# Kernel tuning notes

Hardware: AMD Instinct MI355X
Metric: run time of the kernel (lower is better)

Reference implementation:

```python
import jax, jax.numpy as jnp
import numpy as np

CTX, H, ENC, BALL = 256, 128, 128, 2
IN_DIM = 2 + BALL + ENC  # prev_disp(2) + ball(2) + encoding(128)
B, T = 8192, 128


def setup_inputs() -> dict:
    key = jax.random.key(0)
    ks = jax.random.split(key, 16)
    s = lambda fan_in: 1.0 / np.sqrt(fan_in)
    inp = {
        "context": jax.random.normal(ks[0], (B, CTX), jnp.float32),
        "target_encoding": jax.random.normal(ks[1], (B, ENC), jnp.float32),
        "ball_land_xy": jax.random.normal(ks[2], (B, BALL), jnp.float32),
        "max_frames": T,
        # context_to_h / context_to_c
        "Wh": jax.random.uniform(ks[3], (H, CTX), jnp.float32, -s(CTX), s(CTX)),
        "bh": jax.random.uniform(ks[4], (H,), jnp.float32, -s(CTX), s(CTX)),
        "Wc": jax.random.uniform(ks[5], (H, CTX), jnp.float32, -s(CTX), s(CTX)),
        "bc": jax.random.uniform(ks[6], (H,), jnp.float32, -s(CTX), s(CTX)),
        # LSTM (PyTorch gate order: i, f, g, o)
        "W_ih": jax.random.uniform(ks[7], (4 * H, IN_DIM), jnp.float32, -s(H), s(H)),
        "W_hh": jax.random.uniform(ks[8], (4 * H, H), jnp.float32, -s(H), s(H)),
        "b_ih": jax.random.uniform(ks[9], (4 * H,), jnp.float32, -s(H), s(H)),
        "b_hh": jax.random.uniform(ks[10], (4 * H,), jnp.float32, -s(H), s(H)),
        # output head
        "Wo": jax.random.uniform(ks[11], (2, H), jnp.float32, -s(H), s(H)),
        "bo": jax.random.uniform(ks[12], (2,), jnp.float32, -s(H), s(H)),
    }
    return inp


def _decode(context, target_encoding, ball_land_xy, Wh, bh, Wc, bc,
            W_ih, W_hh, b_ih, b_hh, Wo, bo, max_frames):
    h0 = context @ Wh.T + bh                      # (B, H)
    c0 = context @ Wc.T + bc                      # (B, H)
    Bn = context.shape[0]
    # split input weights: first 2 cols act on prev_disp, rest on static [ball, enc]
    W_prev = W_ih[:, :2]                          # (4H, 2)
    W_stat = W_ih[:, 2:]                          # (4H, BALL+ENC)
    static_in = jnp.concatenate([ball_land_xy, target_encoding], axis=-1)
    gate_static = static_in @ W_stat.T + b_ih + b_hh  # (B, 4H), constant per step
    Hn = h0.shape[-1]

    def step(carry, _):
        h, c, prev = carry
        gates = prev @ W_prev.T + h @ W_hh.T + gate_static
        i, f, g, o = jnp.split(gates, 4, axis=-1)
        c = jax.nn.sigmoid(f) * c + jax.nn.sigmoid(i) * jnp.tanh(g)
        h = jax.nn.sigmoid(o) * jnp.tanh(c)
        pred = h @ Wo.T + bo                      # (B, 2)
        prev = jax.lax.stop_gradient(pred)        # matches .detach()
        return (h, c, prev), pred

    prev0 = jnp.zeros((Bn, 2), dtype=context.dtype)
    _, preds = jax.lax.scan(step, (h0, c0, prev0), None, length=max_frames)
    return jnp.transpose(preds, (1, 0, 2))        # (B, T, 2)


def reference(context, target_encoding, ball_land_xy, max_frames,
              Wh, bh, Wc, bc, W_ih, W_hh, b_ih, b_hh, Wo, bo):
    return _decode(context, target_encoding, ball_land_xy, Wh, bh, Wc, bc,
                   W_ih, W_hh, b_ih, b_hh, Wo, bo, max_frames)
```

## Files before the change

### kernel.cpp

```cpp
#include <hip/hip_runtime.h>
#include <hip/hip_bf16.h>


#define HDIM 128
#define CTX_DIM 256
#define T_FRAMES 128
#define BB 32
#define STR 136

typedef __bf16 bf16x8 __attribute__((ext_vector_type(8)));
typedef float  f32x4  __attribute__((ext_vector_type(4)));

union frag_u {
  bf16x8 v;
  unsigned short s[8];
  uint4 u4;
};

#if __has_builtin(__builtin_amdgcn_exp2f)
#define EXP2(x) __builtin_amdgcn_exp2f(x)
#else
#define EXP2(x) __expf((x) * 0.6931471805599453f)
#endif
#define RCP(x) __builtin_amdgcn_rcpf(x)

__device__ __forceinline__ unsigned short f2bf(float x) {
  unsigned u = __builtin_bit_cast(unsigned, x);
  u += 0x7FFFu + ((u >> 16) & 1u);
  return (unsigned short)(u >> 16);
}
__device__ __forceinline__ float bf2f(unsigned short h) {
  unsigned u = ((unsigned)h) << 16;
  return __builtin_bit_cast(float, u);
}
template<int CTRL>
__device__ __forceinline__ float dpp_mov(float x) {
  return __builtin_bit_cast(float,
    __builtin_amdgcn_mov_dpp(__builtin_bit_cast(int, x), CTRL, 0xF, 0xF, true));
}
__device__ __forceinline__ float row_reduce16(float v) {
  v += dpp_mov<0xB1>(v);
  v += dpp_mov<0x4E>(v);
  v += dpp_mov<0x124>(v);
  v += dpp_mov<0x128>(v);
  return v;
}

template<int N> struct Int { static constexpr int value = N; };

#define MFMA(a, b, c) __builtin_amdgcn_mfma_f32_16x16x32_bf16((a), (b), (c), 0, 0, 0)

__global__ __launch_bounds__(512, 1) void traj_lstm(
    const float* __restrict__ ctx, const float* __restrict__ enc,
    const float* __restrict__ ball,
    const float* __restrict__ Wh, const float* __restrict__ bh,
    const float* __restrict__ Wc, const float* __restrict__ bc,
    const float* __restrict__ W_ih, const float* __restrict__ W_hh,
    const float* __restrict__ b_ih, const float* __restrict__ b_hh,
    const float* __restrict__ Wo, const float* __restrict__ bo,
    float* __restrict__ outp)
{
  __shared__ __align__(16) __bf16 sh_h[2][BB * STR];
  __shared__ __align__(16) unsigned short sh_sA[BB * 264];
  __shared__ __align__(16) unsigned short sh_sB[BB * 264];
  __shared__ __align__(16) uint4 sh_wof[4 * 64];
  __shared__ float sh_pw0[8][BB * 2];
  __shared__ float sh_p0[BB * 2];

  const int tid  = threadIdx.x;
  const int w    = tid >> 6;
  const int l    = tid & 63;
  const int q    = l >> 4;
  const int c16  = l & 15;
  const int colH = w * 16 + c16;
  const int rbase = blockIdx.x * BB;

  const float Lc = 1.4426950408889634f;
  const float SG[4] = {Lc, Lc, 2.f * Lc, Lc};
  const float bo0 = bo[0], bo1 = bo[1];
  const float wo0 = Wo[colH], wo1 = Wo[HDIM + colH];

  float wp0[4], wp1[4];
  #pragma unroll
  for (int g = 0; g < 4; ++g) {
    wp0[g] = W_ih[(size_t)(g * HDIM + colH) * 132 + 0];
    wp1[g] = W_ih[(size_t)(g * HDIM + colH) * 132 + 1];
  }

  frag_u Wf[4][4];
  #pragma unroll
  for (int kt = 0; kt < 4; ++kt) {
    const float* w0p = Wo + kt * 32 + q * 8;
    const float* w1p = Wo + HDIM + kt * 32 + q * 8;
    float4 a0 = *(const float4*)w0p, a1 = *(const float4*)(w0p + 4);
    float4 b0 = *(const float4*)w1p, b1 = *(const float4*)(w1p + 4);
    float wo0v[8] = {a0.x, a0.y, a0.z, a0.w, a1.x, a1.y, a1.z, a1.w};
    float wo1v[8] = {b0.x, b0.y, b0.z, b0.w, b1.x, b1.y, b1.z, b1.w};
    #pragma unroll
    for (int g = 0; g < 4; ++g) {
      const float* wr = W_hh + (size_t)(g * HDIM + colH) * HDIM + kt * 32 + q * 8;
      float4 f0 = *(const float4*)wr;
      float4 f1 = *(const float4*)(wr + 4);
      float ff[8] = {f0.x, f0.y, f0.z, f0.w, f1.x, f1.y, f1.z, f1.w};
      #pragma unroll
      for (int j = 0; j < 8; ++j)
        Wf[g][kt].s[j] = f2bf(SG[g] * (ff[j] + wp0[g] * wo0v[j] + wp1[g] * wo1v[j]));
    }
  }

  #pragma unroll
  for (int kt = 0; kt < 4; ++kt) {
    frag_u wf;
    #pragma unroll
    for (int j = 0; j < 8; ++j) {
      float x = (c16 < 2) ? Wo[c16 * HDIM + kt * 32 + q * 8 + j] : 0.f;
      wf.s[j] = f2bf(x);
    }
    if (w == 0) sh_wof[kt * 64 + l] = wf.u4;
  }

  for (int e = tid; e < BB * 256; e += 512) {
    int row = e >> 8, col = e & 255;
    float x = ctx[(size_t)(rbase + row) * CTX_DIM + col];
    unsigned short hb = f2bf(x);
    sh_sA[row * 264 + col] = hb;
    sh_sB[row * 264 + col] = f2bf(x - bf2f(hb));
  }
  __syncthreads();

  float cst[2][4];
  {
    f32x4 aH[2] = {{0.f,0.f,0.f,0.f},{0.f,0.f,0.f,0.f}};
    f32x4 aC[2] = {{0.f,0.f,0.f,0.f},{0.f,0.f,0.f,0.f}};
    #pragma unroll
    for (int kt = 0; kt < 8; ++kt) {
      frag_u Ahi[2], Alo[2];
      #pragma unroll
      for (int rt = 0; rt < 2; ++rt) {
        Ahi[rt].u4 = *(const uint4*)&sh_sA[(rt * 16 + c16) * 264 + kt * 32 + q * 8];
        Alo[rt].u4 = *(const uint4*)&sh_sB[(rt * 16 + c16) * 264 + kt * 32 + q * 8];
      }
      frag_u bhi, blo;
      {
        const float* wr = Wh + (size_t)colH * CTX_DIM + kt * 32 + q * 8;
        float4 f0 = *(const float4*)wr;
        float4 f1 = *(const float4*)(wr + 4);
        float ff[8] = {f0.x, f0.y, f0.z, f0.w, f1.x, f1.y, f1.z, f1.w};
        #pragma unroll
        for (int j = 0; j < 8; ++j) {
          unsigned short hb = f2bf(ff[j]);
          bhi.s[j] = hb;
          blo.s[j] = f2bf(ff[j] - bf2f(hb));
        }
      }
      #pragma unroll
      for (int rt = 0; rt < 2; ++rt) {
        aH[rt] = MFMA(Ahi[rt].v, bhi.v, aH[rt]);
        aH[rt] = MFMA(Alo[rt].v, bhi.v, aH[rt]);
        aH[rt] = MFMA(Ahi[rt].v, blo.v, aH[rt]);
      }
      {
        const float* wr = Wc + (size_t)colH * CTX_DIM + kt * 32 + q * 8;
        float4 f0 = *(const float4*)wr;
        float4 f1 = *(const float4*)(wr + 4);
        float ff[8] = {f0.x, f0.y, f0.z, f0.w, f1.x, f1.y, f1.z, f1.w};
        #pragma unroll
        for (int j = 0; j < 8; ++j) {
          unsigned short hb = f2bf(ff[j]);
          bhi.s[j] = hb;
          blo.s[j] = f2bf(ff[j] - bf2f(hb));
        }
      }
      #pragma unroll
      for (int rt = 0; rt < 2; ++rt) {
        aC[rt] = MFMA(Ahi[rt].v, bhi.v, aC[rt]);
        aC[rt] = MFMA(Alo[rt].v, bhi.v, aC[rt]);
        aC[rt] = MFMA(Ahi[rt].v, blo.v, aC[rt]);
      }
    }
    float bhv = bh[colH], bcv = bc[colH];
    float pp0[8][2];
    #pragma unroll
    for (int rt = 0; rt < 2; ++rt) {
      #pragma unroll
      for (int r = 0; r < 4; ++r) {
        float h0v = aH[rt][r] + bhv;
        cst[rt][r] = aC[rt][r] + bcv;
        sh_h[0][(rt * 16 + q * 4 + r) * STR + colH] = (__bf16)h0v;
        pp0[rt * 4 + r][0] = h0v * wo0;
        pp0[rt * 4 + r][1] = h0v * wo1;
      }
    }
    #pragma unroll
    for (int m = 0; m < 8; ++m) {
      pp0[m][0] = row_reduce16(pp0[m][0]);
      pp0[m][1] = row_reduce16(pp0[m][1]);
    }
    if (c16 == 0) {
      #pragma unroll
      for (int rt = 0; rt < 2; ++rt)
        #pragma unroll
        for (int r = 0; r < 4; ++r) {
          sh_pw0[w][(rt * 16 + q * 4 + r) * 2 + 0] = pp0[rt * 4 + r][0];
          sh_pw0[w][(rt * 16 + q * 4 + r) * 2 + 1] = pp0[rt * 4 + r][1];
        }
    }
  }
  __syncthreads();

  for (int e = tid; e < BB * 168; e += 512) {
    int row = e / 168, col = e - row * 168;
    float x = (col < 2) ? ball[(size_t)(rbase + row) * 2 + col]
            : (col < 130) ? enc[(size_t)(rbase + row) * 128 + (col - 2)] : 0.f;
    unsigned short hb = f2bf(x);
    sh_sA[row * 168 + col] = hb;
    sh_sB[row * 168 + col] = f2bf(x - bf2f(hb));
  }
  if (tid < BB * 2) {
    float s = (tid & 1) ? bo1 : bo0;
    #pragma unroll
    for (int w2 = 0; w2 < 8; ++w2) s += sh_pw0[w2][tid];
    sh_p0[tid] = s;
  }
  __syncthreads();

  f32x4 gacc[2][4] = {{{0.f,0.f,0.f,0.f},{0.f,0.f,0.f,0.f},{0.f,0.f,0.f,0.f},{0.f,0.f,0.f,0.f}},
                      {{0.f,0.f,0.f,0.f},{0.f,0.f,0.f,0.f},{0.f,0.f,0.f,0.f},{0.f,0.f,0.f,0.f}}};
  #pragma unroll
  for (int kt = 0; kt < 5; ++kt) {
    frag_u Ahi[2], Alo[2];
    #pragma unroll
    for (int rt = 0; rt < 2; ++rt) {
      Ahi[rt].u4 = *(const uint4*)&sh_sA[(rt * 16 + c16) * 168 + kt * 32 + q * 8];
      Alo[rt].u4 = *(const uint4*)&sh_sB[(rt * 16 + c16) * 168 + kt * 32 + q * 8];
    }
    #pragma unroll
    for (int g = 0; g < 4; ++g) {
      frag_u bhi, blo;
      #pragma unroll
      for (int j = 0; j < 8; ++j) {
        int kk = kt * 32 + q * 8 + j;
        float x = (kk < 130) ? SG[g] * W_ih[(size_t)(g * HDIM + colH) * 132 + 2 + kk] : 0.f;
        unsigned short hb = f2bf(x);
        bhi.s[j] = hb;
        blo.s[j] = f2bf(x - bf2f(hb));
      }
      #pragma unroll
      for (int rt = 0; rt < 2; ++rt) {
        gacc[rt][g] = MFMA(Ahi[rt].v, bhi.v, gacc[rt][g]);
        gacc[rt][g] = MFMA(Alo[rt].v, bhi.v, gacc[rt][g]);
        gacc[rt][g] = MFMA(Ahi[rt].v, blo.v, gacc[rt][g]);
      }
    }
  }
  float wps0[4], wps1[4];
  #pragma unroll
  for (int g = 0; g < 4; ++g) {
    int colG = g * HDIM + colH;
    float bb = SG[g] * (b_ih[colG] + b_hh[colG] + bo0 * wp0[g] + bo1 * wp1[g]);
    #pragma unroll
    for (int rt = 0; rt < 2; ++rt)
      #pragma unroll
      for (int r = 0; r < 4; ++r) gacc[rt][g][r] += bb;
    wps0[g] = SG[g] * wp0[g];
    wps1[g] = SG[g] * wp1[g];
  }

  f32x4 acc[2][4];

  auto phase = [&](auto GC, int t, bool doEw, bool corr, bool doPred) {
    constexpr int G = decltype(GC)::value;
    constexpr int E = 1 - G;
    const int rbuf = t & 1;
    const __bf16* hp = &sh_h[rbuf][(G * 16 + c16) * STR];

    frag_u A[4];
    #pragma unroll
    for (int kt = 0; kt < 4; ++kt)
      A[kt].u4 = *(const uint4*)(hp + kt * 32 + q * 8);
    #pragma unroll
    for (int g = 0; g < 4; ++g) acc[G][g] = gacc[G][g];
    #pragma unroll
    for (int kt = 0; kt < 4; ++kt)
      #pragma unroll
      for (int g = 0; g < 4; ++g)
        acc[G][g] = MFMA(A[kt].v, Wf[g][kt].v, acc[G][g]);

    if (doPred && w == 6 + G) {
      f32x4 accP = {0.f, 0.f, 0.f, 0.f};
      #pragma unroll
      for (int kt = 0; kt < 4; ++kt) {
        frag_u wof;
        wof.u4 = sh_wof[kt * 64 + l];
        accP = MFMA(A[kt].v, wof.v, accP);
      }
      if (c16 < 2) {
        const int m0 = G * 16 + q * 4;
        const float bov = c16 ? bo1 : bo0;
        #pragma unroll
        for (int r = 0; r < 4; ++r)
          outp[(size_t)(rbase + m0 + r) * (T_FRAMES * 2) + (t - 1) * 2 + c16] = accP[r] + bov;
      }
    }

    if (doEw) {
      if (corr) {
        #pragma unroll
        for (int r = 0; r < 4; ++r) {
          float2 p0r = *(const float2*)&sh_p0[(E * 16 + q * 4 + r) * 2];
          #pragma unroll
          for (int g = 0; g < 4; ++g)
            acc[E][g][r] -= p0r.x * wps0[g] + p0r.y * wps1[g];
        }
      }
      __bf16* hwp = &sh_h[(t + G) & 1][(E * 16) * STR + colH];
      #pragma unroll
      for (int r = 0; r < 4; ++r) {
        float ei = EXP2(-acc[E][0][r]);
        float ef = EXP2(-acc[E][1][r]);
        float eg = EXP2(-acc[E][2][r]);
        float eo = EXP2(-acc[E][3][r]);
        float t1 = (1.f + ei) * (1.f + eg);
        float pf = 1.f + ef;
        float num = cst[E][r] * t1 + (1.f - eg) * pf;
        float cv = num * RCP(t1 * pf);
        cst[E][r] = cv;
        float cc = fmaxf(cv, -15.f);
        float ec = EXP2(cc * (-2.f * 1.4426950408889634f));
        float hv = (1.f - ec) * RCP((1.f + eo) * (1.f + ec));
        hwp[(q * 4 + r) * STR] = (__bf16)hv;
      }
    }
    __syncthreads();
  };

  phase(Int<0>{}, 0, false, false, false);
  phase(Int<1>{}, 0, true,  true,  false);
  phase(Int<0>{}, 1, true,  true,  true);
  for (int t = 1; t < 127; ++t) {
    phase(Int<1>{}, t,     true, false, true);
    phase(Int<0>{}, t + 1, true, false, true);
  }
  phase(Int<1>{}, 127, true, false, true);

  {
    __bf16* hwp = &sh_h[0][16 * STR + colH];
    #pragma unroll
    for (int r = 0; r < 4; ++r) {
      float ei = EXP2(-acc[1][0][r]);
      float ef = EXP2(-acc[1][1][r]);
      float eg = EXP2(-acc[1][2][r]);
      float eo = EXP2(-acc[1][3][r]);
      float t1 = (1.f + ei) * (1.f + eg);
      float pf = 1.f + ef;
      float num = cst[1][r] * t1 + (1.f - eg) * pf;
      float cv = num * RCP(t1 * pf);
      float cc = fmaxf(cv, -15.f);
      float ec = EXP2(cc * (-2.f * 1.4426950408889634f));
      float hv = (1.f - ec) * RCP((1.f + eo) * (1.f + ec));
      hwp[(q * 4 + r) * STR] = (__bf16)hv;
    }
  }
  __syncthreads();

  if (w == 6 || w == 7) {
    const int Ge = w - 6;
    const __bf16* hp = &sh_h[0][(Ge * 16 + c16) * STR];
    f32x4 accP = {0.f, 0.f, 0.f, 0.f};
    #pragma unroll
    for (int kt = 0; kt < 4; ++kt) {
      frag_u A, wof;
      A.u4 = *(const uint4*)(hp + kt * 32 + q * 8);
      wof.u4 = sh_wof[kt * 64 + l];
      accP = MFMA(A.v, wof.v, accP);
    }
    if (c16 < 2) {
      const int m0 = Ge * 16 + q * 4;
      const float bov = c16 ? bo1 : bo0;
      #pragma unroll
      for (int r = 0; r < 4; ++r)
        outp[(size_t)(rbase + m0 + r) * (T_FRAMES * 2) + 127 * 2 + c16] = accP[r] + bov;
    }
  }
}

extern "C" void kernel_launch(void* const* d_in, const int* in_sizes, int n_in,
                              void* d_out, int out_size, void* d_ws, size_t ws_size,
                              hipStream_t stream) {
  (void)in_sizes; (void)n_in; (void)d_ws; (void)ws_size; (void)out_size;
  const float* ctx  = (const float*)d_in[0];
  const float* enc  = (const float*)d_in[1];
  const float* ball = (const float*)d_in[2];
  const float* Wh   = (const float*)d_in[4];
  const float* bh   = (const float*)d_in[5];
  const float* Wc   = (const float*)d_in[6];
  const float* bc   = (const float*)d_in[7];
  const float* W_ih = (const float*)d_in[8];
  const float* W_hh = (const float*)d_in[9];
  const float* b_ih = (const float*)d_in[10];
  const float* b_hh = (const float*)d_in[11];
  const float* Wo   = (const float*)d_in[12];
  const float* bo   = (const float*)d_in[13];
  float* outp = (float*)d_out;

  dim3 grid(256), block(512);
  traj_lstm<<<grid, block, 0, stream>>>(ctx, enc, ball, Wh, bh, Wc, bc,
                                        W_ih, W_hh, b_ih, b_hh, Wo, bo, outp);
}
```

Baseline: 307.1 us.

## Specialize waves into MFMA producers and elementwise consumers via LDS gate buffers

Splits the 8 waves of each block by role. Waves 0-3 hold twice the W_hh fragments and compute all gate MFMAs for one 16-row half, writing the gate sums to padded LDS buffers. Waves 4-7 read those sums, add the static gate term and run the LSTM cell math, keeping the cell state in registers. The goal is to overlap matrix and transcendental work across waves, cut per-wave register use so launch_bounds can allow 2 blocks per CU, and reuse the context staging area for the gate buffers. The cost is an extra LDS round trip for the gates at every step, a single h buffer, and load imbalance between the two roles.

```diff
diff --git a/kernel.cpp b/kernel.cpp
--- a/kernel.cpp
+++ b/kernel.cpp
@@ -7,6 +7,7 @@
 #define T_FRAMES 128
 #define BB 32
 #define STR 136
+#define GPAD 129
 
 typedef __bf16 bf16x8 __attribute__((ext_vector_type(8)));
 typedef float  f32x4  __attribute__((ext_vector_type(4)));
@@ -50,7 +51,7 @@
 
 #define MFMA(a, b, c) __builtin_amdgcn_mfma_f32_16x16x32_bf16((a), (b), (c), 0, 0, 0)
 
-__global__ __launch_bounds__(512, 1) void traj_lstm(
+__global__ __launch_bounds__(512, 2) void traj_lstm(
     const float* __restrict__ ctx, const float* __restrict__ enc,
     const float* __restrict__ ball,
     const float* __restrict__ Wh, const float* __restrict__ bh,
@@ -60,12 +61,18 @@
     const float* __restrict__ Wo, const float* __restrict__ bo,
     float* __restrict__ outp)
 {
-  __shared__ __align__(16) __bf16 sh_h[2][BB * STR];
-  __shared__ __align__(16) unsigned short sh_sA[BB * 264];
-  __shared__ __align__(16) unsigned short sh_sB[BB * 264];
+  __shared__ __align__(16) char sh_arena[2 * 16 * GPAD * 16];
+  __shared__ __align__(16) float sh_cb[BB * HDIM];
+  __shared__ __align__(16) __bf16 sh_h[BB * STR];
   __shared__ __align__(16) uint4 sh_wof[4 * 64];
   __shared__ float sh_pw0[8][BB * 2];
   __shared__ float sh_p0[BB * 2];
+
+  unsigned short* sh_sA = (unsigned short*)sh_arena;
+  unsigned short* sh_sB = sh_sA + BB * 264;
+  f32x4* gs  = (f32x4*)sh_arena;
+  f32x4* gbA = (f32x4*)sh_arena;
+  f32x4* gbB = (f32x4*)(sh_arena + 16 * GPAD * 16);
 
   const int tid  = threadIdx.x;
   const int w    = tid >> 6;
@@ -75,6 +82,9 @@
   const int colH = w * 16 + c16;
   const int rbase = blockIdx.x * BB;
 
+  const int hcE   = ((w - 4) << 5) + (l & 31);
+  const int halfE = l >> 5;
+
   const float Lc = 1.4426950408889634f;
   const float SG[4] = {Lc, Lc, 2.f * Lc, Lc};
   const float bo0 = bo[0], bo1 = bo[1];
@@ -85,27 +95,6 @@
   for (int g = 0; g < 4; ++g) {
     wp0[g] = W_ih[(size_t)(g * HDIM + colH) * 132 + 0];
     wp1[g] = W_ih[(size_t)(g * HDIM + colH) * 132 + 1];
-  }
-
-  frag_u Wf[4][4];
-  #pragma unroll
-  for (int kt = 0; kt < 4; ++kt) {
-    const float* w0p = Wo + kt * 32 + q * 8;
-    const float* w1p = Wo + HDIM + kt * 32 + q * 8;
-    float4 a0 = *(const float4*)w0p, a1 = *(const float4*)(w0p + 4);
-    float4 b0 = *(const float4*)w1p, b1 = *(const float4*)(w1p + 4);
-    float wo0v[8] = {a0.x, a0.y, a0.z, a0.w, a1.x, a1.y, a1.z, a1.w};
-    float wo1v[8] = {b0.x, b0.y, b0.z, b0.w, b1.x, b1.y, b1.z, b1.w};
-    #pragma unroll
-    for (int g = 0; g < 4; ++g) {
-      const float* wr = W_hh + (size_t)(g * HDIM + colH) * HDIM + kt * 32 + q * 8;
-      float4 f0 = *(const float4*)wr;
-      float4 f1 = *(const float4*)(wr + 4);
-      float ff[8] = {f0.x, f0.y, f0.z, f0.w, f1.x, f1.y, f1.z, f1.w};
-      #pragma unroll
-      for (int j = 0; j < 8; ++j)
-        Wf[g][kt].s[j] = f2bf(SG[g] * (ff[j] + wp0[g] * wo0v[j] + wp1[g] * wo1v[j]));
-    }
   }
 
   #pragma unroll
@@ -128,7 +117,6 @@
   }
   __syncthreads();
 
-  float cst[2][4];
   {
     f32x4 aH[2] = {{0.f,0.f,0.f,0.f},{0.f,0.f,0.f,0.f}};
     f32x4 aC[2] = {{0.f,0.f,0.f,0.f},{0.f,0.f,0.f,0.f}};
@@ -184,9 +172,10 @@
     for (int rt = 0; rt < 2; ++rt) {
       #pragma unroll
       for (int r = 0; r < 4; ++r) {
+        int row = rt * 16 + q * 4 + r;
         float h0v = aH[rt][r] + bhv;
-        cst[rt][r] = aC[rt][r] + bcv;
-        sh_h[0][(rt * 16 + q * 4 + r) * STR + colH] = (__bf16)h0v;
+        sh_h[row * STR + colH] = (__bf16)h0v;
+        sh_cb[row * HDIM + colH] = aC[rt][r] + bcv;
         pp0[rt * 4 + r][0] = h0v * wo0;
         pp0[rt * 4 + r][1] = h0v * wo1;
       }
@@ -253,7 +242,6 @@
       }
     }
   }
-  float wps0[4], wps1[4];
   #pragma unroll
   for (int g = 0; g < 4; ++g) {
     int colG = g * HDIM + colH;
@@ -262,73 +250,139 @@
     for (int rt = 0; rt < 2; ++rt)
       #pragma unroll
       for (int r = 0; r < 4; ++r) gacc[rt][g][r] += bb;
-    wps0[g] = SG[g] * wp0[g];
-    wps1[g] = SG[g] * wp1[g];
-  }
-
-  f32x4 acc[2][4];
-
-  auto phase = [&](auto GC, int t, bool doEw, bool corr, bool doPred) {
+  }
+  __syncthreads();
+
+  #pragma unroll
+  for (int rt = 0; rt < 2; ++rt)
+    #pragma unroll
+    for (int r = 0; r < 4; ++r) {
+      f32x4 vv = {gacc[rt][0][r], gacc[rt][1][r], gacc[rt][2][r], gacc[rt][3][r]};
+      gs[(rt * 16 + q * 4 + r) * HDIM + colH] = vv;
+    }
+  __syncthreads();
+
+  f32x4 gstatE[2][8];
+  float cstE[2][8];
+  float wpsE0[4], wpsE1[4];
+  frag_u Wf[4][2][4];
+  if (w >= 4) {
+    #pragma unroll
+    for (int G2 = 0; G2 < 2; ++G2)
+      #pragma unroll
+      for (int r = 0; r < 8; ++r) {
+        int row = G2 * 16 + halfE * 8 + r;
+        gstatE[G2][r] = gs[row * HDIM + hcE];
+        cstE[G2][r]   = sh_cb[row * HDIM + hcE];
+      }
+    #pragma unroll
+    for (int g = 0; g < 4; ++g) {
+      wpsE0[g] = SG[g] * W_ih[(size_t)(g * HDIM + hcE) * 132 + 0];
+      wpsE1[g] = SG[g] * W_ih[(size_t)(g * HDIM + hcE) * 132 + 1];
+    }
+  } else {
+    #pragma unroll
+    for (int ctl = 0; ctl < 2; ++ctl) {
+      const int colW = w * 32 + ctl * 16 + c16;
+      float wpA[4], wpB[4];
+      #pragma unroll
+      for (int g = 0; g < 4; ++g) {
+        wpA[g] = W_ih[(size_t)(g * HDIM + colW) * 132 + 0];
+        wpB[g] = W_ih[(size_t)(g * HDIM + colW) * 132 + 1];
+      }
+      #pragma unroll
+      for (int kt = 0; kt < 4; ++kt) {
+        const float* w0p = Wo + kt * 32 + q * 8;
+        const float* w1p = Wo + HDIM + kt * 32 + q * 8;
+        float4 a0 = *(const float4*)w0p, a1 = *(const float4*)(w0p + 4);
+        float4 b0 = *(const float4*)w1p, b1 = *(const float4*)(w1p + 4);
+        float wo0v[8] = {a0.x, a0.y, a0.z, a0.w, a1.x, a1.y, a1.z, a1.w};
+        float wo1v[8] = {b0.x, b0.y, b0.z, b0.w, b1.x, b1.y, b1.z, b1.w};
+        #pragma unroll
+        for (int g = 0; g < 4; ++g) {
+          const float* wr = W_hh + (size_t)(g * HDIM + colW) * HDIM + kt * 32 + q * 8;
+          float4 f0 = *(const float4*)wr;
+          float4 f1 = *(const float4*)(wr + 4);
+          float ff[8] = {f0.x, f0.y, f0.z, f0.w, f1.x, f1.y, f1.z, f1.w};
+          #pragma unroll
+          for (int j = 0; j < 8; ++j)
+            Wf[g][ctl][kt].s[j] = f2bf(SG[g] * (ff[j] + wpA[g] * wo0v[j] + wpB[g] * wo1v[j]));
+        }
+      }
+    }
+  }
+  __syncthreads();
+
+  auto phase = [&](auto GC, int t, bool doEW, bool corr, bool doPred) {
     constexpr int G = decltype(GC)::value;
     constexpr int E = 1 - G;
-    const int rbuf = t & 1;
-    const __bf16* hp = &sh_h[rbuf][(G * 16 + c16) * STR];
-
-    frag_u A[4];
-    #pragma unroll
-    for (int kt = 0; kt < 4; ++kt)
-      A[kt].u4 = *(const uint4*)(hp + kt * 32 + q * 8);
-    #pragma unroll
-    for (int g = 0; g < 4; ++g) acc[G][g] = gacc[G][g];
-    #pragma unroll
-    for (int kt = 0; kt < 4; ++kt)
+    if (w < 4) {
+      frag_u A[4];
+      #pragma unroll
+      for (int kt = 0; kt < 4; ++kt)
+        A[kt].u4 = *(const uint4*)&sh_h[(G * 16 + c16) * STR + kt * 32 + q * 8];
+      f32x4 acc[4][2];
       #pragma unroll
       for (int g = 0; g < 4; ++g)
-        acc[G][g] = MFMA(A[kt].v, Wf[g][kt].v, acc[G][g]);
-
-    if (doPred && w == 6 + G) {
-      f32x4 accP = {0.f, 0.f, 0.f, 0.f};
-      #pragma unroll
-      for (int kt = 0; kt < 4; ++kt) {
-        frag_u wof;
-        wof.u4 = sh_wof[kt * 64 + l];
-        accP = MFMA(A[kt].v, wof.v, accP);
-      }
-      if (c16 < 2) {
-        const int m0 = G * 16 + q * 4;
-        const float bov = c16 ? bo1 : bo0;
-        #pragma unroll
-        for (int r = 0; r < 4; ++r)
-          outp[(size_t)(rbase + m0 + r) * (T_FRAMES * 2) + (t - 1) * 2 + c16] = accP[r] + bov;
-      }
-    }
-
-    if (doEw) {
-      if (corr) {
+        #pragma unroll
+        for (int ctl = 0; ctl < 2; ++ctl)
+          acc[g][ctl] = (f32x4){0.f, 0.f, 0.f, 0.f};
+      #pragma unroll
+      for (int kt = 0; kt < 4; ++kt)
+        #pragma unroll
+        for (int g = 0; g < 4; ++g)
+          #pragma unroll
+          for (int ctl = 0; ctl < 2; ++ctl)
+            acc[g][ctl] = MFMA(A[kt].v, Wf[g][ctl][kt].v, acc[g][ctl]);
+      f32x4* gb = (G == 0) ? gbA : gbB;
+      #pragma unroll
+      for (int ctl = 0; ctl < 2; ++ctl)
         #pragma unroll
         for (int r = 0; r < 4; ++r) {
-          float2 p0r = *(const float2*)&sh_p0[(E * 16 + q * 4 + r) * 2];
+          f32x4 vv = {acc[0][ctl][r], acc[1][ctl][r], acc[2][ctl][r], acc[3][ctl][r]};
+          gb[(q * 4 + r) * GPAD + (w * 32 + ctl * 16 + c16)] = vv;
+        }
+      if (doPred && w == 0) {
+        f32x4 accP = {0.f, 0.f, 0.f, 0.f};
+        #pragma unroll
+        for (int kt = 0; kt < 4; ++kt) {
+          frag_u wof;
+          wof.u4 = sh_wof[kt * 64 + l];
+          accP = MFMA(A[kt].v, wof.v, accP);
+        }
+        if (c16 < 2) {
+          const float bov = c16 ? bo1 : bo0;
+          #pragma unroll
+          for (int r = 0; r < 4; ++r)
+            outp[(size_t)(rbase + G * 16 + q * 4 + r) * (T_FRAMES * 2) + (t - 1) * 2 + c16] = accP[r] + bov;
+        }
+      }
+    } else if (doEW) {
+      f32x4* gb = (E == 0) ? gbA : gbB;
+      #pragma unroll
+      for (int r = 0; r < 8; ++r) {
+        const int row = halfE * 8 + r;
+        f32x4 gt = gb[row * GPAD + hcE];
+        gt += gstatE[E][r];
+        if (corr) {
+          float2 p0r = *(const float2*)&sh_p0[(E * 16 + row) * 2];
           #pragma unroll
           for (int g = 0; g < 4; ++g)
-            acc[E][g][r] -= p0r.x * wps0[g] + p0r.y * wps1[g];
-        }
-      }
-      __bf16* hwp = &sh_h[(t + G) & 1][(E * 16) * STR + colH];
-      #pragma unroll
-      for (int r = 0; r < 4; ++r) {
-        float ei = EXP2(-acc[E][0][r]);
-        float ef = EXP2(-acc[E][1][r]);
-        float eg = EXP2(-acc[E][2][r]);
-        float eo = EXP2(-acc[E][3][r]);
+            gt[g] -= p0r.x * wpsE0[g] + p0r.y * wpsE1[g];
+        }
+        float ei = EXP2(-gt[0]);
+        float ef = EXP2(-gt[1]);
+        float eg = EXP2(-gt[2]);
+        float eo = EXP2(-gt[3]);
         float t1 = (1.f + ei) * (1.f + eg);
         float pf = 1.f + ef;
-        float num = cst[E][r] * t1 + (1.f - eg) * pf;
+        float num = cstE[E][r] * t1 + (1.f - eg) * pf;
         float cv = num * RCP(t1 * pf);
-        cst[E][r] = cv;
+        cstE[E][r] = cv;
         float cc = fmaxf(cv, -15.f);
         float ec = EXP2(cc * (-2.f * 1.4426950408889634f));
         float hv = (1.f - ec) * RCP((1.f + eo) * (1.f + ec));
-        hwp[(q * 4 + r) * STR] = (__bf16)hv;
+        sh_h[(E * 16 + row) * STR + hcE] = (__bf16)hv;
       }
     }
     __syncthreads();
@@ -337,49 +391,51 @@
   phase(Int<0>{}, 0, false, false, false);
   phase(Int<1>{}, 0, true,  true,  false);
   phase(Int<0>{}, 1, true,  true,  true);
-  for (int t = 1; t < 127; ++t) {
-    phase(Int<1>{}, t,     true, false, true);
-    phase(Int<0>{}, t + 1, true, false, true);
-  }
-  phase(Int<1>{}, 127, true, false, true);
-
-  {
-    __bf16* hwp = &sh_h[0][16 * STR + colH];
-    #pragma unroll
-    for (int r = 0; r < 4; ++r) {
-      float ei = EXP2(-acc[1][0][r]);
-      float ef = EXP2(-acc[1][1][r]);
-      float eg = EXP2(-acc[1][2][r]);
-      float eo = EXP2(-acc[1][3][r]);
+  phase(Int<1>{}, 1, true,  false, true);
+  for (int t = 2; t <= 127; ++t) {
+    phase(Int<0>{}, t, true, false, true);
+    phase(Int<1>{}, t, true, false, true);
+  }
+
+  if (w >= 4) {
+    #pragma unroll
+    for (int r = 0; r < 8; ++r) {
+      const int row = halfE * 8 + r;
+      f32x4 gt = gbB[row * GPAD + hcE];
+      gt += gstatE[1][r];
+      float ei = EXP2(-gt[0]);
+      float ef = EXP2(-gt[1]);
+      float eg = EXP2(-gt[2]);
+      float eo = EXP2(-gt[3]);
       float t1 = (1.f + ei) * (1.f + eg);
       float pf = 1.f + ef;
-      float num = cst[1][r] * t1 + (1.f - eg) * pf;
+      float num = cstE[1][r] * t1 + (1.f - eg) * pf;
       float cv = num * RCP(t1 * pf);
       float cc = fmaxf(cv, -15.f);
       float ec = EXP2(cc * (-2.f * 1.4426950408889634f));
       float hv = (1.f - ec) * RCP((1.f + eo) * (1.f + ec));
-      hwp[(q * 4 + r) * STR] = (__bf16)hv;
-    }
-  }
-  __syncthreads();
-
-  if (w == 6 || w == 7) {
-    const int Ge = w - 6;
-    const __bf16* hp = &sh_h[0][(Ge * 16 + c16) * STR];
-    f32x4 accP = {0.f, 0.f, 0.f, 0.f};
-    #pragma unroll
-    for (int kt = 0; kt < 4; ++kt) {
-      frag_u A, wof;
-      A.u4 = *(const uint4*)(hp + kt * 32 + q * 8);
-      wof.u4 = sh_wof[kt * 64 + l];
-      accP = MFMA(A.v, wof.v, accP);
-    }
-    if (c16 < 2) {
-      const int m0 = Ge * 16 + q * 4;
-      const float bov = c16 ? bo1 : bo0;
-      #pragma unroll
-      for (int r = 0; r < 4; ++r)
-        outp[(size_t)(rbase + m0 + r) * (T_FRAMES * 2) + 127 * 2 + c16] = accP[r] + bov;
+      sh_h[(16 + row) * STR + hcE] = (__bf16)hv;
+    }
+  }
+  __syncthreads();
+
+  if (w == 0) {
+    #pragma unroll
+    for (int G2 = 0; G2 < 2; ++G2) {
+      f32x4 accP = {0.f, 0.f, 0.f, 0.f};
+      #pragma unroll
+      for (int kt = 0; kt < 4; ++kt) {
+        frag_u A, wof;
+        A.u4 = *(const uint4*)&sh_h[(G2 * 16 + c16) * STR + kt * 32 + q * 8];
+        wof.u4 = sh_wof[kt * 64 + l];
+        accP = MFMA(A.v, wof.v, accP);
+      }
+      if (c16 < 2) {
+        const float bov = c16 ? bo1 : bo0;
+        #pragma unroll
+        for (int r = 0; r < 4; ++r)
+          outp[(size_t)(rbase + G2 * 16 + q * 4 + r) * (T_FRAMES * 2) + 127 * 2 + c16] = accP[r] + bov;
+      }
     }
   }
 }
```

Measured after the change: 479.1 us. 56.0% more time.
